# Optimization experiments

Hardware: AMD Instinct MI355X
Metric: run time of the kernel (lower is better)

Reference implementation:

```python
import jax, jax.numpy as jnp
import numpy as np

B, T, C, H = 2, 2048, 1024, 16  # head_dim for V = C//H = 64; QK head dim = 3


def setup_inputs() -> dict:
    key = jax.random.key(0)
    ks = jax.random.split(key, 6)
    x = jax.random.normal(ks[0], (B, T, C), dtype=jnp.float32)
    wq = jax.random.normal(ks[1], (C, H * 3), dtype=jnp.float32) * (C ** -0.5)
    wk = jax.random.normal(ks[2], (C, H * 3), dtype=jnp.float32) * (C ** -0.5)
    wv = jax.random.normal(ks[3], (C, C), dtype=jnp.float32) * (C ** -0.5)
    wo = jax.random.normal(ks[4], (C, C), dtype=jnp.float32) * (C ** -0.5)
    dirs = jax.random.normal(ks[5], (H, 3), dtype=jnp.float32)
    head_dirs = dirs / jnp.linalg.norm(dirs, axis=1, keepdims=True)  # unit trigram dirs
    scale = jnp.full((1,), 1.0 / np.sqrt(3.0), dtype=jnp.float32)
    return {"x": x, "wq": wq, "wk": wk, "wv": wv, "wo": wo,
            "head_dirs": head_dirs, "scale": scale}


def reference(x, wq, wk, wv, wo, head_dirs, scale):
    b, t, c = x.shape
    h = head_dirs.shape[0]
    hd = c // h
    # projections: QK live in a 3-dim geometric space per head
    q3 = (x @ wq).reshape(b, t, h, 3).transpose(0, 2, 1, 3)   # (B,H,T,3)
    k3 = (x @ wk).reshape(b, t, h, 3).transpose(0, 2, 1, 3)   # (B,H,T,3)
    v = (x @ wv).reshape(b, t, h, hd).transpose(0, 2, 1, 3)   # (B,H,T,hd)
    # projections of q,k onto per-head trigram directions
    q_on_dir = jnp.einsum('bhtd,hd->bht', q3, head_dirs)      # (B,H,T)
    k_on_dir = jnp.einsum('bhtd,hd->bht', k3, head_dirs)      # (B,H,T)
    dot_scores = jnp.einsum('bhtd,bhsd->bhts', q3, k3) * scale  # (B,H,T,T)
    geo_bias = q_on_dir[..., :, None] * k_on_dir[..., None, :]  # outer product bias
    scores = dot_scores + geo_bias
    causal = jnp.tril(jnp.ones((t, t), dtype=bool))
    scores = jnp.where(causal, scores, -jnp.inf)
    attn = jax.nn.softmax(scores, axis=-1)  # dropout p=0 -> identity
    out = jnp.einsum('bhts,bhsd->bhtd', attn, v)
    out = out.transpose(0, 2, 1, 3).reshape(b, t, c)
    return out @ wo
```

## Files before the change

kernel.cpp:

```cpp
#include <hip/hip_runtime.h>
#include <hip/hip_bf16.h>


typedef short bf16x8 __attribute__((ext_vector_type(8)));
typedef float f32x4 __attribute__((ext_vector_type(4)));
typedef __hip_bfloat16 bf16_t;
typedef unsigned int __attribute__((address_space(1))) u32_as1;
typedef unsigned int __attribute__((address_space(3))) u32_as3;

#define T_SEQ 2048
#define NHEAD 16
#define CDIM 1024

__device__ __forceinline__ void gl_lds16(const void* g, void* l) {
  __builtin_amdgcn_global_load_lds((const u32_as1*)g, (u32_as3*)l, 16, 0, 0);
}

__device__ __forceinline__ f32x4 mfma16(bf16x8 a, bf16x8 b, f32x4 c) {
  return __builtin_amdgcn_mfma_f32_16x16x32_bf16(a, b, c, 0, 0, 0);
}

__device__ __forceinline__ unsigned short f2bf(float f) {
  __hip_bfloat16 h = __float2bfloat16(f);
  return *(unsigned short*)&h;
}

__global__ __launch_bounds__(256) void k_prep(const float* __restrict__ x,
                                              const float* __restrict__ wq,
                                              const float* __restrict__ wk,
                                              const float* __restrict__ wv,
                                              const float* __restrict__ wo,
                                              bf16_t* __restrict__ xb,
                                              bf16_t* __restrict__ wqkT,
                                              bf16_t* __restrict__ wvT,
                                              bf16_t* __restrict__ woT) {
  __shared__ bf16_t tile[32][33];
  int bid = blockIdx.x, tid = threadIdx.x;
  if (bid < 4096) {
    int i = bid * 256 + tid;
    float4 v = ((const float4*)x)[i];
    ushort4 o;
    o.x = f2bf(v.x); o.y = f2bf(v.y); o.z = f2bf(v.z); o.w = f2bf(v.w);
    ((ushort4*)xb)[i] = o;
    return;
  }
  const float* src; bf16_t* dst; int R, C, bx, by;
  if (bid < 5120)      { int t = bid - 4096; src = wv; dst = wvT;            R = 1024; C = 1024; bx = t & 31; by = t >> 5; }
  else if (bid < 6144) { int t = bid - 5120; src = wo; dst = woT;            R = 1024; C = 1024; bx = t & 31; by = t >> 5; }
  else if (bid < 6208) { int t = bid - 6144; src = wq; dst = wqkT;           R = 1024; C = 48;   bx = t & 1;  by = t >> 1; }
  else                 { int t = bid - 6208; src = wk; dst = wqkT + 48*1024; R = 1024; C = 48;   bx = t & 1;  by = t >> 1; }
  int tx = tid & 31, ty = tid >> 5;
  int r0 = by * 32, c0 = bx * 32;
#pragma unroll
  for (int j = 0; j < 32; j += 8) {
    int r = r0 + ty + j, c = c0 + tx;
    if (r < R && c < C) tile[ty + j][tx] = __float2bfloat16(src[(size_t)r * C + c]);
  }
  __syncthreads();
#pragma unroll
  for (int j = 0; j < 32; j += 8) {
    int c = c0 + ty + j, r = r0 + tx;
    if (r < R && c < C) dst[(size_t)c * R + r] = tile[tx][ty + j];
  }
}

__global__ __launch_bounds__(256) void k_qkproj(const bf16_t* __restrict__ xb,
                                                const bf16_t* __restrict__ wqkT,
                                                const float* __restrict__ head_dirs,
                                                const float* __restrict__ scale,
                                                float* __restrict__ Qt,
                                                float* __restrict__ Kt) {
  __shared__ float red[4][16][96];
  int tid = threadIdx.x, wave = tid >> 6, lane = tid & 63;
  int g = lane >> 4, li = lane & 15;
  int m0 = blockIdx.x * 16;
  f32x4 acc[6] = {};
  int kb = wave * 256;
  for (int k0 = kb; k0 < kb + 256; k0 += 32) {
    bf16x8 a = *(const bf16x8*)(xb + (size_t)(m0 + li) * 1024 + k0 + g * 8);
#pragma unroll
    for (int nt = 0; nt < 6; ++nt) {
      bf16x8 bb = *(const bf16x8*)(wqkT + (size_t)(nt * 16 + li) * 1024 + k0 + g * 8);
      acc[nt] = mfma16(a, bb, acc[nt]);
    }
  }
#pragma unroll
  for (int nt = 0; nt < 6; ++nt)
#pragma unroll
    for (int r = 0; r < 4; ++r) red[wave][g * 4 + r][nt * 16 + li] = acc[nt][r];
  __syncthreads();
  for (int i = tid; i < 16 * 96; i += 256) {
    int row = i / 96, col = i - (i / 96) * 96;
    float v = red[0][row][col] + red[1][row][col] + red[2][row][col] + red[3][row][col];
    if (col >= 48) {
      int n = col - 48;
      int h = n / 3, c = n - h * 3;
      int mg = m0 + row;
      int bb = mg >> 11, tt = mg & 2047;
      Kt[(((size_t)bb * NHEAD + h) * 3 + c) * T_SEQ + tt] = v;
    } else {
      red[0][row][col] = v;
    }
  }
  __syncthreads();
  int row = tid >> 4, h = tid & 15;
  float q0 = red[0][row][h * 3 + 0];
  float q1 = red[0][row][h * 3 + 1];
  float q2 = red[0][row][h * 3 + 2];
  float d0 = head_dirs[h * 3 + 0];
  float d1 = head_dirs[h * 3 + 1];
  float d2 = head_dirs[h * 3 + 2];
  float sc = scale[0];
  float dot = q0 * d0 + q1 * d1 + q2 * d2;
  int mg = m0 + row;
  int bb = mg >> 11, tt = mg & 2047;
  size_t base = ((size_t)bb * NHEAD + h) * 3 * T_SEQ + tt;
  Qt[base] = sc * q0 + d0 * dot;
  Qt[base + T_SEQ] = sc * q1 + d1 * dot;
  Qt[base + 2 * T_SEQ] = sc * q2 + d2 * dot;
}

__global__ __launch_bounds__(256) void k_gemm_bt(const bf16_t* __restrict__ A,
                                                 const bf16_t* __restrict__ Bt,
                                                 void* __restrict__ Cout,
                                                 int M, int N, int K, int mode) {
  __shared__ alignas(16) bf16_t As[64 * 32];
  __shared__ alignas(16) bf16_t Bs[128 * 32];
  int tid = threadIdx.x, wave = tid >> 6, lane = tid & 63;
  int g = lane >> 4, li = lane & 15;
  int n0 = blockIdx.x * 128, m0 = blockIdx.y * 64;
  int wm = wave >> 1, wn = wave & 1;

  const bf16_t* gA0 = A + (size_t)(m0 + (tid >> 2)) * K + (tid & 3) * 8;
  const bf16_t* gB0 = Bt + (size_t)(n0 + (tid >> 2)) * K + (tid & 3) * 8;
  const bf16_t* gB1 = Bt + (size_t)(n0 + 64 + (tid >> 2)) * K + (tid & 3) * 8;
  char* lA = (char*)As + (size_t)(wave * 64) * 16;
  char* lB0 = (char*)Bs + (size_t)(wave * 64) * 16;
  char* lB1 = (char*)Bs + (size_t)(256 + wave * 64) * 16;

  f32x4 acc[2][4] = {};

  for (int k0 = 0; k0 < K; k0 += 32) {
    __syncthreads();
    gl_lds16(gA0 + k0, lA);
    gl_lds16(gB0 + k0, lB0);
    gl_lds16(gB1 + k0, lB1);
    __syncthreads();
    bf16x8 af[2], bfr[4];
#pragma unroll
    for (int mt = 0; mt < 2; ++mt)
      af[mt] = *(const bf16x8*)&As[(wm * 32 + mt * 16 + li) * 32 + g * 8];
#pragma unroll
    for (int nt = 0; nt < 4; ++nt)
      bfr[nt] = *(const bf16x8*)&Bs[(wn * 64 + nt * 16 + li) * 32 + g * 8];
#pragma unroll
    for (int mt = 0; mt < 2; ++mt)
#pragma unroll
      for (int nt = 0; nt < 4; ++nt)
        acc[mt][nt] = mfma16(af[mt], bfr[nt], acc[mt][nt]);
  }

#pragma unroll
  for (int mt = 0; mt < 2; ++mt)
#pragma unroll
    for (int nt = 0; nt < 4; ++nt)
#pragma unroll
      for (int r = 0; r < 4; ++r) {
        int m = m0 + wm * 32 + mt * 16 + g * 4 + r;
        int n = n0 + wn * 64 + nt * 16 + li;
        float v = acc[mt][nt][r];
        if (mode == 0) {
          int bb = n >> 11, tt = n & 2047;
          ((bf16_t*)Cout)[((size_t)bb * 1024 + m) * T_SEQ + tt] = __float2bfloat16(v);
        } else {
          ((float*)Cout)[(size_t)m * N + n] = v;
        }
      }
}

__global__ __launch_bounds__(256) void k_attn(const float* __restrict__ Qt,
                                              const float* __restrict__ Kt,
                                              const bf16_t* __restrict__ VT,
                                              bf16_t* __restrict__ att) {
  __shared__ alignas(16) bf16_t Vb[2][64 * 64];
  int tid = threadIdx.x, wave = tid >> 6, lane = tid & 63;
  int g = lane >> 4, li = lane & 15;
  int bid = blockIdx.x;
  int qt = 31 - (bid >> 5);
  int bh = bid & 31;
  int b = bh >> 4, h = bh & 15;
  int mw = wave * 16;

  const float* Qp = Qt + (size_t)bh * 3 * T_SEQ;
  const float* Kp = Kt + (size_t)bh * 3 * T_SEQ;
  const bf16_t* Vp = VT + (size_t)bh * 64 * T_SEQ;

  int tq = qt * 64 + mw + li;
  float q0 = Qp[tq], q1 = Qp[T_SEQ + tq], q2 = Qp[2 * T_SEQ + tq];

  bf16x8 bones;
  unsigned short ob = (li == 0) ? (unsigned short)0x3F80 : (unsigned short)0;
#pragma unroll
  for (int j = 0; j < 8; ++j) bones[j] = (short)ob;

  const bf16_t* vg[2];
#pragma unroll
  for (int p = 0; p < 2; ++p) {
    int P = p * 256 + wave * 64 + lane;
    int d = P >> 3, c = (P & 7) ^ (d & 7);
    vg[p] = Vp + (size_t)d * T_SEQ + c * 8;
  }
  char* vl0[2] = {(char*)&Vb[0][0] + wave * 64 * 16, (char*)&Vb[1][0] + wave * 64 * 16};
  char* vl1[2] = {(char*)&Vb[0][0] + (256 + wave * 64) * 16,
                  (char*)&Vb[1][0] + (256 + wave * 64) * 16};

  f32x4 kreg[2][3][2];
#define LOAD_K(s0)                                                        \
  {                                                                       \
    _Pragma("unroll") for (int half = 0; half < 2; ++half) {              \
      const float* kp = Kp + (s0) + half * 32 + g * 8;                    \
      _Pragma("unroll") for (int c = 0; c < 3; ++c) {                     \
        kreg[half][c][0] = *(const f32x4*)(kp + c * T_SEQ);               \
        kreg[half][c][1] = *(const f32x4*)(kp + c * T_SEQ + 4);           \
      }                                                                   \
    }                                                                     \
  }

  LOAD_K(0);
  gl_lds16(vg[0], vl0[0]);
  gl_lds16(vg[1], vl1[0]);

  f32x4 acc[5] = {};
  int sw = li & 7;

  for (int st = 0; st <= qt; ++st) {
    int buf = st & 1;
    __syncthreads();
    if (st < qt) {
      int s1 = (st + 1) * 64;
      gl_lds16(vg[0] + s1, vl0[buf ^ 1]);
      gl_lds16(vg[1] + s1, vl1[buf ^ 1]);
    }
    bf16x8 afrag[2];
    bool diag = (st == qt);
#pragma unroll
    for (int half = 0; half < 2; ++half)
#pragma unroll
      for (int j = 0; j < 8; ++j) {
        float kk0 = kreg[half][0][j >> 2][j & 3];
        float kk1 = kreg[half][1][j >> 2][j & 3];
        float kk2 = kreg[half][2][j >> 2][j & 3];
        float scv = q0 * kk0 + q1 * kk1 + q2 * kk2;
        float pv = __expf(fminf(scv, 80.0f));
        if (diag && (half * 32 + g * 8 + j > mw + li)) pv = 0.0f;
        afrag[half][j] = (short)f2bf(pv);
      }
    if (st < qt) LOAD_K((st + 1) * 64);
    const bf16_t* vb = &Vb[buf][0];
#pragma unroll
    for (int nt = 0; nt < 4; ++nt) {
      int row = nt * 16 + li;
      bf16x8 b0 = *(const bf16x8*)&vb[row * 64 + (g ^ sw) * 8];
      bf16x8 b1 = *(const bf16x8*)&vb[row * 64 + ((4 + g) ^ sw) * 8];
      acc[nt] = mfma16(afrag[0], b0, acc[nt]);
      acc[nt] = mfma16(afrag[1], b1, acc[nt]);
    }
    acc[4] = mfma16(afrag[0], bones, acc[4]);
    acc[4] = mfma16(afrag[1], bones, acc[4]);
  }

  float linv[4];
#pragma unroll
  for (int r = 0; r < 4; ++r)
    linv[r] = 1.0f / fmaxf(__shfl(acc[4][r], lane & 48), 1e-35f);

#pragma unroll
  for (int nt = 0; nt < 4; ++nt)
#pragma unroll
    for (int r = 0; r < 4; ++r) {
      int t = qt * 64 + mw + g * 4 + r;
      att[((size_t)b * T_SEQ + t) * CDIM + h * 64 + nt * 16 + li] =
          __float2bfloat16(acc[nt][r] * linv[r]);
    }
}

extern "C" void kernel_launch(void* const* d_in, const int* in_sizes, int n_in,
                              void* d_out, int out_size, void* d_ws, size_t ws_size,
                              hipStream_t stream) {
  const float* x  = (const float*)d_in[0];
  const float* wq = (const float*)d_in[1];
  const float* wk = (const float*)d_in[2];
  const float* wv = (const float*)d_in[3];
  const float* wo = (const float*)d_in[4];
  const float* hd = (const float*)d_in[5];
  const float* sc = (const float*)d_in[6];
  float* out = (float*)d_out;

  char* ws = (char*)d_ws;
  bf16_t* wqkT = (bf16_t*)(ws + 0);
  bf16_t* wvT  = (bf16_t*)(ws + 196608);
  bf16_t* woT  = (bf16_t*)(ws + 2293760);
  float*  Qt   = (float*)(ws + 4390912);
  float*  Kt   = (float*)(ws + 5177344);
  bf16_t* VT   = (bf16_t*)(ws + 5963776);
  bf16_t* att  = (bf16_t*)(ws + 14352384);
  bf16_t* xb   = (bf16_t*)(ws + 22740992);

  k_prep<<<6272, 256, 0, stream>>>(x, wq, wk, wv, wo, xb, wqkT, wvT, woT);

  k_qkproj<<<256, 256, 0, stream>>>(xb, wqkT, hd, sc, Qt, Kt);

  k_gemm_bt<<<dim3(32, 16), 256, 0, stream>>>(wvT, xb, VT, 1024, 4096, 1024, 0);

  k_attn<<<1024, 256, 0, stream>>>(Qt, Kt, VT, att);

  k_gemm_bt<<<dim3(8, 64), 256, 0, stream>>>(att, woT, out, 4096, 1024, 1024, 1);
}
```

Measured before the change: 179.1 us.

## Double-buffer GEMM LDS, stage K through LDS in 128-key attention steps

The GEMM now double-buffers its A/B LDS tiles, prefetching the next k-slice before computing the current one, which removes one barrier per iteration. The attention kernel loads K through LDS with global_load_lds alongside V, processes 128 keys per barrier as two 64-key sub-tiles, and skips sub-tiles that lie entirely above the causal diagonal. The log2(e) factor is folded into Q during prep so the kernel can call the hardware exp2 directly. The cost is more LDS per block, which may reduce occupancy, plus an occupancy hint in the launch bounds.

```diff
diff --git a/kernel.cpp b/kernel.cpp
--- a/kernel.cpp
+++ b/kernel.cpp
@@ -11,6 +11,7 @@
 #define T_SEQ 2048
 #define NHEAD 16
 #define CDIM 1024
+#define L2E 1.4426950408889634f
 
 __device__ __forceinline__ void gl_lds16(const void* g, void* l) {
   __builtin_amdgcn_global_load_lds((const u32_as1*)g, (u32_as3*)l, 16, 0, 0);
@@ -23,6 +24,14 @@
 __device__ __forceinline__ unsigned short f2bf(float f) {
   __hip_bfloat16 h = __float2bfloat16(f);
   return *(unsigned short*)&h;
+}
+
+__device__ __forceinline__ float fast_exp2(float x) {
+#if __has_builtin(__builtin_amdgcn_exp2f)
+  return __builtin_amdgcn_exp2f(x);
+#else
+  return exp2f(x);
+#endif
 }
 
 __global__ __launch_bounds__(256) void k_prep(const float* __restrict__ x,
@@ -110,8 +119,8 @@
   float d0 = head_dirs[h * 3 + 0];
   float d1 = head_dirs[h * 3 + 1];
   float d2 = head_dirs[h * 3 + 2];
-  float sc = scale[0];
-  float dot = q0 * d0 + q1 * d1 + q2 * d2;
+  float sc = scale[0] * L2E;
+  float dot = (q0 * d0 + q1 * d1 + q2 * d2) * L2E;
   int mg = m0 + row;
   int bb = mg >> 11, tt = mg & 2047;
   size_t base = ((size_t)bb * NHEAD + h) * 3 * T_SEQ + tt;
@@ -124,8 +133,8 @@
                                                  const bf16_t* __restrict__ Bt,
                                                  void* __restrict__ Cout,
                                                  int M, int N, int K, int mode) {
-  __shared__ alignas(16) bf16_t As[64 * 32];
-  __shared__ alignas(16) bf16_t Bs[128 * 32];
+  __shared__ alignas(16) bf16_t As[2][64 * 32];
+  __shared__ alignas(16) bf16_t Bs[2][128 * 32];
   int tid = threadIdx.x, wave = tid >> 6, lane = tid & 63;
   int g = lane >> 4, li = lane & 15;
   int n0 = blockIdx.x * 128, m0 = blockIdx.y * 64;
@@ -134,31 +143,35 @@
   const bf16_t* gA0 = A + (size_t)(m0 + (tid >> 2)) * K + (tid & 3) * 8;
   const bf16_t* gB0 = Bt + (size_t)(n0 + (tid >> 2)) * K + (tid & 3) * 8;
   const bf16_t* gB1 = Bt + (size_t)(n0 + 64 + (tid >> 2)) * K + (tid & 3) * 8;
-  char* lA = (char*)As + (size_t)(wave * 64) * 16;
-  char* lB0 = (char*)Bs + (size_t)(wave * 64) * 16;
-  char* lB1 = (char*)Bs + (size_t)(256 + wave * 64) * 16;
+
+#define GSTAGE(bufi, kk)                                                        \
+  {                                                                             \
+    gl_lds16(gA0 + (kk), (char*)&As[bufi][0] + (size_t)(wave * 64) * 16);       \
+    gl_lds16(gB0 + (kk), (char*)&Bs[bufi][0] + (size_t)(wave * 64) * 16);       \
+    gl_lds16(gB1 + (kk), (char*)&Bs[bufi][0] + (size_t)(256 + wave * 64) * 16); \
+  }
 
   f32x4 acc[2][4] = {};
+  GSTAGE(0, 0);
 
   for (int k0 = 0; k0 < K; k0 += 32) {
+    int cur = (k0 >> 5) & 1;
     __syncthreads();
-    gl_lds16(gA0 + k0, lA);
-    gl_lds16(gB0 + k0, lB0);
-    gl_lds16(gB1 + k0, lB1);
-    __syncthreads();
+    if (k0 + 32 < K) GSTAGE(cur ^ 1, k0 + 32);
     bf16x8 af[2], bfr[4];
 #pragma unroll
     for (int mt = 0; mt < 2; ++mt)
-      af[mt] = *(const bf16x8*)&As[(wm * 32 + mt * 16 + li) * 32 + g * 8];
+      af[mt] = *(const bf16x8*)&As[cur][(wm * 32 + mt * 16 + li) * 32 + g * 8];
 #pragma unroll
     for (int nt = 0; nt < 4; ++nt)
-      bfr[nt] = *(const bf16x8*)&Bs[(wn * 64 + nt * 16 + li) * 32 + g * 8];
+      bfr[nt] = *(const bf16x8*)&Bs[cur][(wn * 64 + nt * 16 + li) * 32 + g * 8];
 #pragma unroll
     for (int mt = 0; mt < 2; ++mt)
 #pragma unroll
       for (int nt = 0; nt < 4; ++nt)
         acc[mt][nt] = mfma16(af[mt], bfr[nt], acc[mt][nt]);
   }
+#undef GSTAGE
 
 #pragma unroll
   for (int mt = 0; mt < 2; ++mt)
@@ -178,11 +191,12 @@
       }
 }
 
-__global__ __launch_bounds__(256) void k_attn(const float* __restrict__ Qt,
-                                              const float* __restrict__ Kt,
-                                              const bf16_t* __restrict__ VT,
-                                              bf16_t* __restrict__ att) {
-  __shared__ alignas(16) bf16_t Vb[2][64 * 64];
+__global__ __launch_bounds__(256, 4) void k_attn(const float* __restrict__ Qt,
+                                                 const float* __restrict__ Kt,
+                                                 const bf16_t* __restrict__ VT,
+                                                 bf16_t* __restrict__ att) {
+  __shared__ alignas(16) bf16_t Vb[2][2][64 * 64];
+  __shared__ alignas(16) float Ks[2][3 * 128];
   int tid = threadIdx.x, wave = tid >> 6, lane = tid & 63;
   int g = lane >> 4, li = lane & 15;
   int bid = blockIdx.x;
@@ -210,64 +224,70 @@
     int d = P >> 3, c = (P & 7) ^ (d & 7);
     vg[p] = Vp + (size_t)d * T_SEQ + c * 8;
   }
-  char* vl0[2] = {(char*)&Vb[0][0] + wave * 64 * 16, (char*)&Vb[1][0] + wave * 64 * 16};
-  char* vl1[2] = {(char*)&Vb[0][0] + (256 + wave * 64) * 16,
-                  (char*)&Vb[1][0] + (256 + wave * 64) * 16};
-
-  f32x4 kreg[2][3][2];
-#define LOAD_K(s0)                                                        \
-  {                                                                       \
-    _Pragma("unroll") for (int half = 0; half < 2; ++half) {              \
-      const float* kp = Kp + (s0) + half * 32 + g * 8;                    \
-      _Pragma("unroll") for (int c = 0; c < 3; ++c) {                     \
-        kreg[half][c][0] = *(const f32x4*)(kp + c * T_SEQ);               \
-        kreg[half][c][1] = *(const f32x4*)(kp + c * T_SEQ + 4);           \
-      }                                                                   \
-    }                                                                     \
-  }
-
-  LOAD_K(0);
-  gl_lds16(vg[0], vl0[0]);
-  gl_lds16(vg[1], vl1[0]);
+  int kch = (wave == 3) ? lane : 32 + lane;
+  const float* kg = Kp + (size_t)(kch >> 5) * T_SEQ + (kch & 31) * 4;
+  int kbase = (wave == 3) ? 0 : 512;
+
+#define STAGE(bufi, s0v)                                                      \
+  {                                                                           \
+    _Pragma("unroll") for (int sub_ = 0; sub_ < 2; ++sub_)                    \
+        _Pragma("unroll") for (int p_ = 0; p_ < 2; ++p_)                      \
+            gl_lds16(vg[p_] + (s0v) + sub_ * 64,                              \
+                     (char*)&Vb[bufi][sub_][0] + (p_ * 256 + wave * 64) * 16);\
+    if (wave >= 2) gl_lds16(kg + (s0v), (char*)&Ks[bufi][0] + kbase);         \
+  }
+
+#define BUILD_AFRAG(MASKED)                                                   \
+  _Pragma("unroll") for (int half = 0; half < 2; ++half) {                    \
+    int kb = sub * 64 + half * 32 + g * 8;                                    \
+    f32x4 kv[3][2];                                                           \
+    _Pragma("unroll") for (int c = 0; c < 3; ++c) {                           \
+      kv[c][0] = *(const f32x4*)(ks + c * 128 + kb);                          \
+      kv[c][1] = *(const f32x4*)(ks + c * 128 + kb + 4);                      \
+    }                                                                         \
+    _Pragma("unroll") for (int j = 0; j < 8; ++j) {                           \
+      float scv = q0 * kv[0][j >> 2][j & 3] + q1 * kv[1][j >> 2][j & 3] +     \
+                  q2 * kv[2][j >> 2][j & 3];                                  \
+      float pv = fast_exp2(fminf(scv, 115.4f));                               \
+      if (MASKED && (bkg + half * 32 + g * 8 + j > tq)) pv = 0.0f;            \
+      afrag[half][j] = (short)f2bf(pv);                                       \
+    }                                                                         \
+  }
+
+  int NT = (qt + 2) >> 1;
+  STAGE(0, 0);
 
   f32x4 acc[5] = {};
   int sw = li & 7;
-
-  for (int st = 0; st <= qt; ++st) {
+  int qmin = qt * 64 + mw;
+  int qmax = qmin + 15;
+
+  for (int st = 0; st < NT; ++st) {
     int buf = st & 1;
     __syncthreads();
-    if (st < qt) {
-      int s1 = (st + 1) * 64;
-      gl_lds16(vg[0] + s1, vl0[buf ^ 1]);
-      gl_lds16(vg[1] + s1, vl1[buf ^ 1]);
+    if (st + 1 < NT) STAGE(buf ^ 1, (st + 1) * 128);
+    const float* ks = &Ks[buf][0];
+#pragma unroll
+    for (int sub = 0; sub < 2; ++sub) {
+      int bkg = st * 128 + sub * 64;
+      if (bkg > qmax) continue;
+      bf16x8 afrag[2];
+      if (bkg + 63 > qmin) { BUILD_AFRAG(1) } else { BUILD_AFRAG(0) }
+      const bf16_t* vb = &Vb[buf][sub][0];
+#pragma unroll
+      for (int nt = 0; nt < 4; ++nt) {
+        int row = nt * 16 + li;
+        bf16x8 b0 = *(const bf16x8*)&vb[row * 64 + (g ^ sw) * 8];
+        bf16x8 b1 = *(const bf16x8*)&vb[row * 64 + ((4 + g) ^ sw) * 8];
+        acc[nt] = mfma16(afrag[0], b0, acc[nt]);
+        acc[nt] = mfma16(afrag[1], b1, acc[nt]);
+      }
+      acc[4] = mfma16(afrag[0], bones, acc[4]);
+      acc[4] = mfma16(afrag[1], bones, acc[4]);
     }
-    bf16x8 afrag[2];
-    bool diag = (st == qt);
-#pragma unroll
-    for (int half = 0; half < 2; ++half)
-#pragma unroll
-      for (int j = 0; j < 8; ++j) {
-        float kk0 = kreg[half][0][j >> 2][j & 3];
-        float kk1 = kreg[half][1][j >> 2][j & 3];
-        float kk2 = kreg[half][2][j >> 2][j & 3];
-        float scv = q0 * kk0 + q1 * kk1 + q2 * kk2;
-        float pv = __expf(fminf(scv, 80.0f));
-        if (diag && (half * 32 + g * 8 + j > mw + li)) pv = 0.0f;
-        afrag[half][j] = (short)f2bf(pv);
-      }
-    if (st < qt) LOAD_K((st + 1) * 64);
-    const bf16_t* vb = &Vb[buf][0];
-#pragma unroll
-    for (int nt = 0; nt < 4; ++nt) {
-      int row = nt * 16 + li;
-      bf16x8 b0 = *(const bf16x8*)&vb[row * 64 + (g ^ sw) * 8];
-      bf16x8 b1 = *(const bf16x8*)&vb[row * 64 + ((4 + g) ^ sw) * 8];
-      acc[nt] = mfma16(afrag[0], b0, acc[nt]);
-      acc[nt] = mfma16(afrag[1], b1, acc[nt]);
-    }
-    acc[4] = mfma16(afrag[0], bones, acc[4]);
-    acc[4] = mfma16(afrag[1], bones, acc[4]);
-  }
+  }
+#undef STAGE
+#undef BUILD_AFRAG
 
   float linv[4];
 #pragma unroll
```

Result: faster. 161.2 us (-10.0%).
